# Kernel optimization log

Hardware: AMD Instinct MI355X
Metric: run time of the kernel (lower is better)

## Reference

```python
import jax, jax.numpy as jnp
import numpy as np

B, S, D = 2, 2048, 2048
HQ, HKV = 16, 4
DH = D // HQ            # 128
P = 8192                # GLU projection dim
ROPE_BASE = 10000.0
EPS = 1e-5              # RMSNorm eps


def setup_inputs() -> dict:
    key = jax.random.key(0)
    ks = jax.random.split(key, 9)
    def w(k, shape, scale=0.02):
        return jax.random.normal(k, shape, jnp.float32) * scale
    x = jax.random.normal(ks[0], (B, S, D), jnp.float32)
    # additive causal mask: 0 on/below diagonal, -1e9 above
    causal = jnp.where(jnp.tril(jnp.ones((S, S), bool)), 0.0, -1e9).astype(jnp.float32)
    return dict(
        x=x,
        attention_mask=causal,
        Wq=w(ks[1], (D, D)),
        Wk=w(ks[2], (D, HKV * DH)),
        Wv=w(ks[3], (D, HKV * DH)),
        Wo=w(ks[4], (D, D)),
        Wg=w(ks[5], (D, P)), bg=jnp.zeros((P,), jnp.float32),
        Wu=w(ks[6], (D, P)), bu=jnp.zeros((P,), jnp.float32),
        Wd=w(ks[7], (P, D)), bd=jnp.zeros((D,), jnp.float32),
        g1=jnp.ones((D,), jnp.float32),
        g2=jnp.ones((D,), jnp.float32),
    )


def _rmsnorm(h, g):
    return h * jax.lax.rsqrt(jnp.mean(h * h, axis=-1, keepdims=True) + EPS) * g


def reference(x, attention_mask, Wq, Wk, Wv, Wo, Wg, bg, Wu, bu, Wd, bd, g1, g2):
    b, s, _ = x.shape
    # RoPE tables (half-split / rotate-half convention)
    pos = jnp.arange(s, dtype=jnp.float32)
    inv_freq = ROPE_BASE ** (-jnp.arange(DH // 2, dtype=jnp.float32) * 2.0 / DH)
    ang = pos[:, None] * inv_freq[None, :]          # [s, dh/2]
    cos, sin = jnp.cos(ang), jnp.sin(ang)
    def rope(v):                                    # v: [..., s, dh]
        v1, v2 = jnp.split(v, 2, axis=-1)
        return jnp.concatenate([v1 * cos - v2 * sin, v1 * sin + v2 * cos], axis=-1)

    # --- pre-norm GQA attention sub-block ---
    xn = _rmsnorm(x, g1)
    Q = (xn @ Wq).reshape(b, s, HQ, DH).transpose(0, 2, 1, 3)    # [b,hq,s,dh]
    K = (xn @ Wk).reshape(b, s, HKV, DH).transpose(0, 2, 1, 3)   # [b,g,s,dh]
    V = (xn @ Wv).reshape(b, s, HKV, DH).transpose(0, 2, 1, 3)   # [b,g,s,dh]
    Q, K = rope(Q), rope(K)
    # split q heads: (head group) with group = HKV, head varies slowest
    Qg = Q.reshape(b, HQ // HKV, HKV, s, DH)                     # [b,h,g,s,dh]
    scores = jnp.einsum('bhgsd,bgtd->bhgst', Qg, K) / np.float32(np.sqrt(DH))
    scores = scores + attention_mask                             # broadcast [s,t]
    att = jax.nn.softmax(scores, axis=-1)
    o = jnp.einsum('bhgst,bgtd->bhgsd', att, V)                  # [b,h,g,s,dh]
    o = o.transpose(0, 3, 1, 2, 4).reshape(b, s, D)              # (head group dhead)
    h = x + o @ Wo

    # --- pre-norm GLU (SwiGLU) feedforward sub-block ---
    hn = _rmsnorm(h, g2)
    glu = (jax.nn.silu(hn @ Wg + bg) * (hn @ Wu + bu)) @ Wd + bd
    return h + glu
```

## Files before the change

kernel.cpp:

```cpp
#include <hip/hip_runtime.h>
#include <hip/hip_bf16.h>
#include <stdint.h>

#define S_LEN 2048
#define NROW  4096
#define DQKV  3072

typedef unsigned short u16;
typedef __attribute__((ext_vector_type(8))) short bf16x8;
typedef __attribute__((ext_vector_type(4))) float f32x4;

__device__ __forceinline__ float bf2f(u16 v) {
  unsigned int u = ((unsigned int)v) << 16;
  return __builtin_bit_cast(float, u);
}
__device__ __forceinline__ u16 f2bf(float f) {
  unsigned int u = __builtin_bit_cast(unsigned int, f);
  u += 0x7FFFu + ((u >> 16) & 1u);
  return (u16)(u >> 16);
}
__device__ __forceinline__ void async16(const void* g, void* l) {
  __builtin_amdgcn_global_load_lds(
      (const __attribute__((address_space(1))) unsigned int*)(uintptr_t)g,
      (__attribute__((address_space(3))) unsigned int*)(uintptr_t)l, 16, 0, 0);
}

__global__ __launch_bounds__(256) void transpose_f32_bf16(
    const float* __restrict__ in, u16* __restrict__ out, int R, int C) {
  __shared__ float t[32][33];
  const int bx = blockIdx.x * 32;
  const int by = blockIdx.y * 32;
  const int tx = threadIdx.x, ty = threadIdx.y;
#pragma unroll
  for (int i = 0; i < 32; i += 8)
    t[ty + i][tx] = in[(size_t)(by + ty + i) * C + bx + tx];
  __syncthreads();
#pragma unroll
  for (int i = 0; i < 32; i += 8)
    out[(size_t)(bx + ty + i) * R + by + tx] = f2bf(t[tx][ty + i]);
}

__global__ __launch_bounds__(256) void rope_tables(float* __restrict__ cosT,
                                                   float* __restrict__ sinT) {
  int idx = blockIdx.x * 256 + threadIdx.x;
  int i = idx & 63, s = idx >> 6;
  float inv = powf(10000.0f, -2.0f * (float)i / 128.0f);
  float ang = (float)s * inv;
  cosT[idx] = cosf(ang);
  sinT[idx] = sinf(ang);
}

__global__ __launch_bounds__(256) void rope_apply(u16* __restrict__ QKV,
                                                  const float* __restrict__ cosT,
                                                  const float* __restrict__ sinT) {
  int idx = blockIdx.x * 256 + threadIdx.x;
  int i = idx & 63;
  int h20 = (idx >> 6) % 20;
  int row = idx / (64 * 20);
  int s = row & (S_LEN - 1);
  int col = (h20 < 16) ? (h20 * 128) : (2048 + (h20 - 16) * 128);
  size_t base = (size_t)row * DQKV + col;
  float v1 = bf2f(QKV[base + i]);
  float v2 = bf2f(QKV[base + 64 + i]);
  float c = cosT[s * 64 + i], sn = sinT[s * 64 + i];
  QKV[base + i]      = f2bf(v1 * c - v2 * sn);
  QKV[base + 64 + i] = f2bf(v1 * sn + v2 * c);
}

__global__ __launch_bounds__(256) void rmsnorm_kernel(const float* __restrict__ x,
                                                      const float* __restrict__ g,
                                                      u16* __restrict__ out) {
  const int row = blockIdx.x, tid = threadIdx.x;
  const float* xr = x + (size_t)row * 2048;
  float4 a = ((const float4*)xr)[tid * 2];
  float4 b = ((const float4*)xr)[tid * 2 + 1];
  float ss = a.x*a.x + a.y*a.y + a.z*a.z + a.w*a.w
           + b.x*b.x + b.y*b.y + b.z*b.z + b.w*b.w;
#pragma unroll
  for (int m = 1; m < 64; m <<= 1) ss += __shfl_xor(ss, m, 64);
  __shared__ float red[4];
  if ((tid & 63) == 0) red[tid >> 6] = ss;
  __syncthreads();
  float tot = red[0] + red[1] + red[2] + red[3];
  float rms = rsqrtf(tot * (1.0f / 2048.0f) + 1e-5f);
  const int c = tid * 8;
  float v[8] = {a.x,a.y,a.z,a.w,b.x,b.y,b.z,b.w};
  u16 o[8];
#pragma unroll
  for (int j = 0; j < 8; j++) o[j] = f2bf(v[j] * rms * g[c + j]);
  *(uint4*)(out + (size_t)row * 2048 + c) = *(uint4*)o;
}

template <int BN, int MODE>
__global__ __launch_bounds__(512, 2) void gemm256(
    const u16* __restrict__ A, const u16* __restrict__ Bt,
    int nx, int K, int N,
    const float* __restrict__ bias, const float* __restrict__ res,
    u16* __restrict__ outb, float* __restrict__ outf) {
  constexpr int BSLOT = (BN == 256) ? 16384 : 8192;
  constexpr int NF = BN / 64;
  __shared__ char ldsA[4 * 16384] __attribute__((aligned(16)));
  __shared__ char ldsB[4 * BSLOT] __attribute__((aligned(16)));
  const int t = threadIdx.x;
  const int nwg = gridDim.x;
  const int wg = ((int)blockIdx.x & 7) * (nwg >> 3) + ((int)blockIdx.x >> 3);
  const int m0 = (wg / nx) * 256, n0 = (wg % nx) * BN;
  const int l = t & 63, w = t >> 6;
  const int wm = w >> 2, wn = w & 3;
  const int lr = l & 15, lg = l >> 4;

  const int cA  = (t & 7) ^ ((t >> 3) & 7);
  const int rb  = 2 * (t >> 3) + (cA >> 2);
  const int kcb = (cA & 3) * 16;
  const int t16 = t * 16;
  const char* aS0 = (const char*)A  + ((size_t)(m0 + rb) * K) * 2 + kcb;
  const char* aS1 = aS0 + (size_t)128 * K * 2;
  const char* bS0 = (const char*)Bt + ((size_t)(n0 + rb) * K) * 2 + kcb;
  const char* bS1 = bS0 + (size_t)128 * K * 2;

  const int NT = K >> 5;

  auto STAGE = [&](int kt) {
    const int slot = kt & 3;
    const size_t ko = (size_t)kt * 64;
    char* sA = ldsA + slot * 16384;
    async16(aS0 + ko, sA + t16);
    async16(aS1 + ko, sA + 8192 + t16);
    char* sB = ldsB + slot * BSLOT;
    async16(bS0 + ko, sB + t16);
    if constexpr (BN == 256) async16(bS1 + ko, sB + 8192 + t16);
  };

  STAGE(0); STAGE(1); STAGE(2);

  f32x4 acc[8][NF] = {};
  const int ci  = ((lg + ((lr & 1) << 2)) ^ ((lr >> 1) & 7)) << 4;
  const int aRd = (wm * 64 + (lr >> 1)) * 128 + ci;
  const int bRd = ((BN == 256 ? wn * 32 : wn * 16) + (lr >> 1)) * 128 + ci;

  for (int kt = 0; kt < NT; ++kt) {
    if (kt < NT - 2) {
      if constexpr (BN == 256) asm volatile("s_waitcnt vmcnt(8)" ::: "memory");
      else                     asm volatile("s_waitcnt vmcnt(6)" ::: "memory");
    } else if (kt == NT - 2) {
      if constexpr (BN == 256) asm volatile("s_waitcnt vmcnt(4)" ::: "memory");
      else                     asm volatile("s_waitcnt vmcnt(3)" ::: "memory");
    } else {
      asm volatile("s_waitcnt vmcnt(0)" ::: "memory");
    }
    __builtin_amdgcn_sched_barrier(0);
    __builtin_amdgcn_s_barrier();
    __builtin_amdgcn_sched_barrier(0);
    if (kt + 3 < NT) STAGE(kt + 3);
    const char* sA = ldsA + (kt & 3) * 16384;
    const char* sB = ldsB + (kt & 3) * BSLOT;
    bf16x8 aF[8], bF[NF];
#pragma unroll
    for (int m = 0; m < 8; m++) aF[m] = *(const bf16x8*)(sA + aRd + m * 1024);
#pragma unroll
    for (int n = 0; n < NF; n++) bF[n] = *(const bf16x8*)(sB + bRd + n * 1024);
    __builtin_amdgcn_s_setprio(1);
#pragma unroll
    for (int m = 0; m < 8; m++)
#pragma unroll
      for (int n = 0; n < NF; n++)
        acc[m][n] = __builtin_amdgcn_mfma_f32_16x16x32_bf16(aF[m], bF[n], acc[m][n], 0, 0, 0);
    __builtin_amdgcn_s_setprio(0);
  }

#pragma unroll
  for (int m = 0; m < 8; m++) {
    const int row = m0 + wm * 128 + m * 16 + lg * 4;
#pragma unroll
    for (int n = 0; n < NF; n++) {
      const int col = n0 + wn * (BN / 4) + n * 16 + lr;
      const float bv = bias ? bias[col] : 0.0f;
#pragma unroll
      for (int r = 0; r < 4; r++) {
        const size_t idx = (size_t)(row + r) * N + col;
        float v = acc[m][n][r] + bv;
        if (MODE == 0) outb[idx] = f2bf(v);
        else           outf[idx] = v + res[idx];
      }
    }
  }
}

__global__ __launch_bounds__(512, 2) void swiglu_gemm(
    const u16* __restrict__ A, const u16* __restrict__ Bg, const u16* __restrict__ Bu,
    int nx, int K, const float* __restrict__ bgv, const float* __restrict__ buv,
    u16* __restrict__ out) {
  __shared__ char ldsA[4 * 16384] __attribute__((aligned(16)));
  __shared__ char ldsB[4 * 16384] __attribute__((aligned(16)));
  const int t = threadIdx.x;
  const int nwg = gridDim.x;
  const int wg = ((int)blockIdx.x & 7) * (nwg >> 3) + ((int)blockIdx.x >> 3);
  const int m0 = (wg / nx) * 256, n0 = (wg % nx) * 128;
  const int l = t & 63, w = t >> 6;
  const int wm = w >> 2, wn = w & 3;
  const int lr = l & 15, lg = l >> 4;

  const int cA  = (t & 7) ^ ((t >> 3) & 7);
  const int rb  = 2 * (t >> 3) + (cA >> 2);
  const int kcb = (cA & 3) * 16;
  const int t16 = t * 16;
  const char* aS0 = (const char*)A  + ((size_t)(m0 + rb) * K) * 2 + kcb;
  const char* aS1 = aS0 + (size_t)128 * K * 2;
  const char* gS  = (const char*)Bg + ((size_t)(n0 + rb) * K) * 2 + kcb;
  const char* uS  = (const char*)Bu + ((size_t)(n0 + rb) * K) * 2 + kcb;

  const int NT = K >> 5;

  auto STAGE = [&](int kt) {
    const int slot = kt & 3;
    const size_t ko = (size_t)kt * 64;
    char* sA = ldsA + slot * 16384;
    async16(aS0 + ko, sA + t16);
    async16(aS1 + ko, sA + 8192 + t16);
    char* sB = ldsB + slot * 16384;
    async16(gS + ko, sB + t16);
    async16(uS + ko, sB + 8192 + t16);
  };

  STAGE(0); STAGE(1); STAGE(2);

  f32x4 accg[8][2] = {}, accu[8][2] = {};
  const int ci  = ((lg + ((lr & 1) << 2)) ^ ((lr >> 1) & 7)) << 4;
  const int aRd = (wm * 64 + (lr >> 1)) * 128 + ci;
  const int bRd = (wn * 16 + (lr >> 1)) * 128 + ci;

  for (int kt = 0; kt < NT; ++kt) {
    if (kt < NT - 2)       asm volatile("s_waitcnt vmcnt(8)" ::: "memory");
    else if (kt == NT - 2) asm volatile("s_waitcnt vmcnt(4)" ::: "memory");
    else                   asm volatile("s_waitcnt vmcnt(0)" ::: "memory");
    __builtin_amdgcn_sched_barrier(0);
    __builtin_amdgcn_s_barrier();
    __builtin_amdgcn_sched_barrier(0);
    if (kt + 3 < NT) STAGE(kt + 3);
    const char* sA = ldsA + (kt & 3) * 16384;
    const char* sB = ldsB + (kt & 3) * 16384;
    bf16x8 aF[8], gF[2], uF[2];
#pragma unroll
    for (int m = 0; m < 8; m++) aF[m] = *(const bf16x8*)(sA + aRd + m * 1024);
#pragma unroll
    for (int n = 0; n < 2; n++) {
      gF[n] = *(const bf16x8*)(sB + bRd + n * 1024);
      uF[n] = *(const bf16x8*)(sB + 8192 + bRd + n * 1024);
    }
    __builtin_amdgcn_s_setprio(1);
#pragma unroll
    for (int m = 0; m < 8; m++)
#pragma unroll
      for (int n = 0; n < 2; n++) {
        accg[m][n] = __builtin_amdgcn_mfma_f32_16x16x32_bf16(aF[m], gF[n], accg[m][n], 0, 0, 0);
        accu[m][n] = __builtin_amdgcn_mfma_f32_16x16x32_bf16(aF[m], uF[n], accu[m][n], 0, 0, 0);
      }
    __builtin_amdgcn_s_setprio(0);
  }

#pragma unroll
  for (int m = 0; m < 8; m++) {
    const int row = m0 + wm * 128 + m * 16 + lg * 4;
#pragma unroll
    for (int n = 0; n < 2; n++) {
      const int col = n0 + wn * 32 + n * 16 + lr;
      const float bgc = bgv[col], buc = buv[col];
#pragma unroll
      for (int r = 0; r < 4; r++) {
        float gv = accg[m][n][r] + bgc;
        float uv = accu[m][n][r] + buc;
        float sg = gv / (1.0f + __expf(-gv));
        out[(size_t)(row + r) * 8192 + col] = f2bf(sg * uv);
      }
    }
  }
}

__global__ __launch_bounds__(256) void attn_kernel(const u16* __restrict__ QKV,
                                                   u16* __restrict__ O) {
  const int bid = blockIdx.x;
  const int half = bid >> 8, rr = bid & 255;
  const int bh = rr >> 3, tt = rr & 7;
  const int qtile = half ? (15 - tt) : tt;
  const int b = bh >> 4, hq = bh & 15, g = hq & 3;
  const int q0 = qtile * 128;
  const int tid = threadIdx.x, l = tid & 63, w = tid >> 6;
  const int lr = l & 15, lg = l >> 4;

  __shared__ u16 kT[64 * 128] __attribute__((aligned(16)));
  __shared__ u16 vT[128 * 64] __attribute__((aligned(16)));
  __shared__ u16 pT[4][32 * 72] __attribute__((aligned(16)));

  const float scale = 0.08838834764831845f;

  bf16x8 qF[2][4];
  const int qrow_base = b * S_LEN + q0 + w * 32;
#pragma unroll
  for (int mq = 0; mq < 2; mq++)
#pragma unroll
    for (int kk = 0; kk < 4; kk++)
      qF[mq][kk] = *(const bf16x8*)(QKV + (size_t)(qrow_base + mq * 16 + lr) * DQKV
                                    + hq * 128 + kk * 32 + lg * 8);

  f32x4 o_acc[2][8] = {};
  float m_run[2][4], l_run[2][4];
#pragma unroll
  for (int mq = 0; mq < 2; mq++)
#pragma unroll
    for (int r = 0; r < 4; r++) { m_run[mq][r] = -1e30f; l_run[mq][r] = 0.0f; }

  const int qmin_w = q0 + w * 32;
  const int nt = (q0 + 128) >> 6;

  for (int it = 0; it < nt; ++it) {
    const int t0 = it * 64;
    __syncthreads();
    {
      const int rbase = tid >> 3;
      const int c16 = (tid & 7) * 16;
#pragma unroll
      for (int pass = 0; pass < 2; ++pass) {
        const int r = rbase + pass * 32;
        const u16* src = QKV + (size_t)(b * S_LEN + t0 + r) * DQKV + 2048 + g * 128 + c16;
        const int rk = r & 7;
#pragma unroll
        for (int jj = 0; jj < 2; ++jj) {
          bf16x8 kv = *(const bf16x8*)(src + jj * 8);
          const int chunk = (c16 >> 3) + jj;
          *(bf16x8*)&kT[r * 128 + ((chunk ^ rk) << 3)] = kv;
        }
#pragma unroll
        for (int jj = 0; jj < 2; ++jj) {
          bf16x8 vv = *(const bf16x8*)(src + 512 + jj * 8);
#pragma unroll
          for (int j = 0; j < 8; ++j) {
            const int d = c16 + jj * 8 + j;
            const int key = (d ^ (d >> 4)) & 7;
            vT[d * 64 + (r & 7) + (((r >> 3) ^ key) << 3)] = (u16)vv[j];
          }
        }
      }
    }
    __syncthreads();

    if (t0 <= qmin_w + 31) {
      f32x4 sc[2][4] = {};
#pragma unroll
      for (int mt = 0; mt < 4; mt++) {
        const int tq = mt * 16 + lr;
        const int tk = tq & 7;
#pragma unroll
        for (int kk = 0; kk < 4; kk++) {
          bf16x8 kF = *(const bf16x8*)&kT[tq * 128 + (((kk * 4 + lg) ^ tk) << 3)];
          sc[0][mt] = __builtin_amdgcn_mfma_f32_16x16x32_bf16(qF[0][kk], kF, sc[0][mt], 0, 0, 0);
          sc[1][mt] = __builtin_amdgcn_mfma_f32_16x16x32_bf16(qF[1][kk], kF, sc[1][mt], 0, 0, 0);
        }
      }
      const bool needMask = (t0 + 63 > qmin_w);
#pragma unroll
      for (int mq = 0; mq < 2; mq++)
#pragma unroll
        for (int mt = 0; mt < 4; mt++)
#pragma unroll
          for (int r = 0; r < 4; r++) {
            float v = sc[mq][mt][r] * scale;
            if (needMask) {
              int qg = qmin_w + mq * 16 + lg * 4 + r;
              int tg = t0 + mt * 16 + lr;
              if (tg > qg) v = -1e30f;
            }
            sc[mq][mt][r] = v;
          }
#pragma unroll
      for (int mq = 0; mq < 2; mq++) {
        float al[4];
#pragma unroll
        for (int r = 0; r < 4; r++) {
          float tmax = fmaxf(fmaxf(sc[mq][0][r], sc[mq][1][r]),
                             fmaxf(sc[mq][2][r], sc[mq][3][r]));
#pragma unroll
          for (int m = 1; m < 16; m <<= 1) tmax = fmaxf(tmax, __shfl_xor(tmax, m, 64));
          float mn = fmaxf(m_run[mq][r], tmax);
          float a = __expf(m_run[mq][r] - mn);
          m_run[mq][r] = mn;
          float rs = 0.0f;
#pragma unroll
          for (int mt = 0; mt < 4; mt++) {
            float pv = __expf(sc[mq][mt][r] - mn);
            sc[mq][mt][r] = pv;
            rs += pv;
          }
#pragma unroll
          for (int m = 1; m < 16; m <<= 1) rs += __shfl_xor(rs, m, 64);
          l_run[mq][r] = l_run[mq][r] * a + rs;
          al[r] = a;
        }
#pragma unroll
        for (int n = 0; n < 8; n++)
#pragma unroll
          for (int r = 0; r < 4; r++) o_acc[mq][n][r] *= al[r];
#pragma unroll
        for (int mt = 0; mt < 4; mt++)
#pragma unroll
          for (int r = 0; r < 4; r++)
            pT[w][(mq * 16 + lg * 4 + r) * 72 + mt * 16 + lr] = f2bf(sc[mq][mt][r]);
      }
      bf16x8 pF[2][2];
#pragma unroll
      for (int mq = 0; mq < 2; mq++)
#pragma unroll
        for (int kt = 0; kt < 2; kt++)
          pF[mq][kt] = *(const bf16x8*)&pT[w][(mq * 16 + lr) * 72 + kt * 32 + lg * 8];
#pragma unroll
      for (int kt = 0; kt < 2; kt++)
#pragma unroll
        for (int n = 0; n < 8; n++) {
          const int d = n * 16 + lr;
          const int key = (d ^ (d >> 4)) & 7;
          bf16x8 vF = *(const bf16x8*)&vT[d * 64 + (((kt * 4 + lg) ^ key) << 3)];
          o_acc[0][n] = __builtin_amdgcn_mfma_f32_16x16x32_bf16(pF[0][kt], vF, o_acc[0][n], 0, 0, 0);
          o_acc[1][n] = __builtin_amdgcn_mfma_f32_16x16x32_bf16(pF[1][kt], vF, o_acc[1][n], 0, 0, 0);
        }
    }
  }
#pragma unroll
  for (int mq = 0; mq < 2; mq++)
#pragma unroll
    for (int n = 0; n < 8; n++)
#pragma unroll
      for (int r = 0; r < 4; r++) {
        float v = o_acc[mq][n][r] / l_run[mq][r];
        int row = b * S_LEN + q0 + w * 32 + mq * 16 + lg * 4 + r;
        int col = hq * 128 + n * 16 + lr;
        O[(size_t)row * 2048 + col] = f2bf(v);
      }
}

extern "C" void kernel_launch(void* const* d_in, const int* in_sizes, int n_in,
                              void* d_out, int out_size, void* d_ws, size_t ws_size,
                              hipStream_t stream) {
  const float* x  = (const float*)d_in[0];
  const float* Wq = (const float*)d_in[2];
  const float* Wk = (const float*)d_in[3];
  const float* Wv = (const float*)d_in[4];
  const float* Wo = (const float*)d_in[5];
  const float* Wg = (const float*)d_in[6];
  const float* bg = (const float*)d_in[7];
  const float* Wu = (const float*)d_in[8];
  const float* bu = (const float*)d_in[9];
  const float* Wd = (const float*)d_in[10];
  const float* bd = (const float*)d_in[11];
  const float* g1 = (const float*)d_in[12];
  const float* g2 = (const float*)d_in[13];

  char* p = (char*)d_ws;
  auto alloc = [&](size_t bytes) { char* r = p; p += (bytes + 255) & ~(size_t)255; return r; };
  u16*   BtQKV = (u16*)alloc((size_t)DQKV * 2048 * 2);
  u16*   WoT   = (u16*)alloc((size_t)2048 * 2048 * 2);
  u16*   WgT   = (u16*)alloc((size_t)8192 * 2048 * 2);
  u16*   WuT   = (u16*)alloc((size_t)8192 * 2048 * 2);
  u16*   WdT   = (u16*)alloc((size_t)2048 * 8192 * 2);
  u16*   xn    = (u16*)alloc((size_t)NROW * 2048 * 2);
  u16*   QKV   = (u16*)alloc((size_t)NROW * DQKV * 2);
  u16*   Obuf  = (u16*)alloc((size_t)NROW * 2048 * 2);
  float* h     = (float*)alloc((size_t)NROW * 2048 * 4);
  u16*   gact  = (u16*)alloc((size_t)NROW * 8192 * 2);
  float* cosT  = (float*)alloc((size_t)S_LEN * 64 * 4);
  float* sinT  = (float*)alloc((size_t)S_LEN * 64 * 4);

  dim3 tb(32, 8);
  transpose_f32_bf16<<<dim3(2048/32, 2048/32), tb, 0, stream>>>(Wq, BtQKV,                    2048, 2048);
  transpose_f32_bf16<<<dim3( 512/32, 2048/32), tb, 0, stream>>>(Wk, BtQKV + 2048ull*2048,     2048,  512);
  transpose_f32_bf16<<<dim3( 512/32, 2048/32), tb, 0, stream>>>(Wv, BtQKV + 2560ull*2048,     2048,  512);
  transpose_f32_bf16<<<dim3(2048/32, 2048/32), tb, 0, stream>>>(Wo, WoT,                      2048, 2048);
  transpose_f32_bf16<<<dim3(8192/32, 2048/32), tb, 0, stream>>>(Wg, WgT,                      2048, 8192);
  transpose_f32_bf16<<<dim3(8192/32, 2048/32), tb, 0, stream>>>(Wu, WuT,                      2048, 8192);
  transpose_f32_bf16<<<dim3(2048/32, 8192/32), tb, 0, stream>>>(Wd, WdT,                      8192, 2048);

  rope_tables<<<(S_LEN * 64) / 256, 256, 0, stream>>>(cosT, sinT);

  rmsnorm_kernel<<<NROW, 256, 0, stream>>>(x, g1, xn);

  gemm256<256, 0><<<192, 512, 0, stream>>>(xn, BtQKV, 12, 2048, 3072,
                                           nullptr, nullptr, QKV, nullptr);

  rope_apply<<<(NROW * 20 * 64) / 256, 256, 0, stream>>>(QKV, cosT, sinT);

  attn_kernel<<<512, 256, 0, stream>>>(QKV, Obuf);

  gemm256<128, 1><<<256, 512, 0, stream>>>(Obuf, WoT, 16, 2048, 2048,
                                           nullptr, x, nullptr, h);

  rmsnorm_kernel<<<NROW, 256, 0, stream>>>(h, g2, xn);

  swiglu_gemm<<<1024, 512, 0, stream>>>(xn, WgT, WuT, 64, 2048, bg, bu, gact);

  gemm256<128, 1><<<256, 512, 0, stream>>>(gact, WdT, 16, 8192, 2048,
                                           bd, h, nullptr, (float*)d_out);
}
```

Measured before the change: 829.0 us.

## Restructure GEMM main loops into 8-phase ping-pong pipeline with K=64 tiles

Replaces the 4-slot K=32 software pipeline in the dense and SwiGLU GEMMs with a double-buffered K=64 scheme. Each iteration is split into four phases that interleave LDS fragment reads, barriers, partial async global-to-LDS loads, and MFMA blocks. The aim is to overlap memory traffic with compute more finely and cut per-iteration wait overhead. In exchange it adds many more workgroup barriers per iteration, and the wrap-around prefetch indices load unused data on the final iterations.

Result: no change. 829.3 us (+0.0%).

```diff
diff --git a/kernel.cpp b/kernel.cpp
--- a/kernel.cpp
+++ b/kernel.cpp
@@ -24,6 +24,11 @@
       (const __attribute__((address_space(1))) unsigned int*)(uintptr_t)g,
       (__attribute__((address_space(3))) unsigned int*)(uintptr_t)l, 16, 0, 0);
 }
+#define LGKM0  do { asm volatile("s_waitcnt lgkmcnt(0)" ::: "memory"); \
+                    __builtin_amdgcn_sched_barrier(0); } while (0)
+#define VMC(n) do { asm volatile("s_waitcnt vmcnt(" #n ")" ::: "memory"); \
+                    __builtin_amdgcn_sched_barrier(0); } while (0)
+#define BAR()  __builtin_amdgcn_s_barrier()
 
 __global__ __launch_bounds__(256) void transpose_f32_bf16(
     const float* __restrict__ in, u16* __restrict__ out, int R, int C) {
@@ -92,15 +97,15 @@
 }
 
 template <int BN, int MODE>
-__global__ __launch_bounds__(512, 2) void gemm256(
+__global__ __launch_bounds__(512, 2) void gemm8p(
     const u16* __restrict__ A, const u16* __restrict__ Bt,
     int nx, int K, int N,
     const float* __restrict__ bias, const float* __restrict__ res,
     u16* __restrict__ outb, float* __restrict__ outf) {
-  constexpr int BSLOT = (BN == 256) ? 16384 : 8192;
   constexpr int NF = BN / 64;
-  __shared__ char ldsA[4 * 16384] __attribute__((aligned(16)));
-  __shared__ char ldsB[4 * BSLOT] __attribute__((aligned(16)));
+  constexpr int BB = BN * 128;
+  __shared__ char ldsA[2 * 32768] __attribute__((aligned(16)));
+  __shared__ char ldsB[2 * BB]    __attribute__((aligned(16)));
   const int t = threadIdx.x;
   const int nwg = gridDim.x;
   const int wg = ((int)blockIdx.x & 7) * (nwg >> 3) + ((int)blockIdx.x >> 3);
@@ -109,63 +114,106 @@
   const int wm = w >> 2, wn = w & 3;
   const int lr = l & 15, lg = l >> 4;
 
-  const int cA  = (t & 7) ^ ((t >> 3) & 7);
-  const int rb  = 2 * (t >> 3) + (cA >> 2);
-  const int kcb = (cA & 3) * 16;
+  const size_t K2 = (size_t)K * 2;
+  const int pr = t >> 3;
+  const int ckb = ((t & 7) ^ (pr & 7)) * 16;
   const int t16 = t * 16;
-  const char* aS0 = (const char*)A  + ((size_t)(m0 + rb) * K) * 2 + kcb;
-  const char* aS1 = aS0 + (size_t)128 * K * 2;
-  const char* bS0 = (const char*)Bt + ((size_t)(n0 + rb) * K) * 2 + kcb;
-  const char* bS1 = bS0 + (size_t)128 * K * 2;
-
-  const int NT = K >> 5;
-
-  auto STAGE = [&](int kt) {
-    const int slot = kt & 3;
-    const size_t ko = (size_t)kt * 64;
-    char* sA = ldsA + slot * 16384;
-    async16(aS0 + ko, sA + t16);
-    async16(aS1 + ko, sA + 8192 + t16);
-    char* sB = ldsB + slot * BSLOT;
-    async16(bS0 + ko, sB + t16);
-    if constexpr (BN == 256) async16(bS1 + ko, sB + 8192 + t16);
+  const char* aSrc = (const char*)A  + (size_t)(m0 + pr) * K2 + ckb;
+  const char* bSrc = (const char*)Bt + (size_t)(n0 + pr) * K2 + ckb;
+
+  auto ST_A = [&](int q, int kt, int buf) {
+    char* d = ldsA + buf * 32768 + q * 16384 + t16;
+    const char* s = aSrc + (size_t)(q * 128) * K2 + (size_t)kt * 128;
+    async16(s, d);
+    async16(s + (size_t)64 * K2, d + 8192);
   };
-
-  STAGE(0); STAGE(1); STAGE(2);
+  auto ST_B = [&](int h, int kt, int buf) {
+    if constexpr (BN == 256) {
+      char* d = ldsB + buf * 32768 + h * 16384 + t16;
+      const char* s = bSrc + (size_t)(h * 128) * K2 + (size_t)kt * 128;
+      async16(s, d);
+      async16(s + (size_t)64 * K2, d + 8192);
+    } else {
+      char* d = ldsB + buf * 16384 + h * 8192 + t16;
+      const char* s = bSrc + (size_t)(h * 64) * K2 + (size_t)kt * 128;
+      async16(s, d);
+    }
+  };
+
+  const int NT = K >> 6;
+  ST_A(0, 0, 0); ST_A(1, 0, 0); ST_B(0, 0, 0); ST_B(1, 0, 0);
+  ST_A(0, 1, 1); ST_A(1, 1, 1);
+  VMC(4);
+  BAR();
+
+  const int key = lr & 7;
+  const int c0 = (lg ^ key) * 16;
+  const int c1 = ((4 + lg) ^ key) * 16;
+  const int aB = wm * 16384 + lr * 128;
+  const int bB = (BN == 256) ? ((wn >> 1) * 16384 + ((wn & 1) * 64 + lr) * 128)
+                             : ((wn >> 1) * 8192  + ((wn & 1) * 32 + lr) * 128);
 
   f32x4 acc[8][NF] = {};
-  const int ci  = ((lg + ((lr & 1) << 2)) ^ ((lr >> 1) & 7)) << 4;
-  const int aRd = (wm * 64 + (lr >> 1)) * 128 + ci;
-  const int bRd = ((BN == 256 ? wn * 32 : wn * 16) + (lr >> 1)) * 128 + ci;
 
   for (int kt = 0; kt < NT; ++kt) {
-    if (kt < NT - 2) {
-      if constexpr (BN == 256) asm volatile("s_waitcnt vmcnt(8)" ::: "memory");
-      else                     asm volatile("s_waitcnt vmcnt(6)" ::: "memory");
-    } else if (kt == NT - 2) {
-      if constexpr (BN == 256) asm volatile("s_waitcnt vmcnt(4)" ::: "memory");
-      else                     asm volatile("s_waitcnt vmcnt(3)" ::: "memory");
-    } else {
-      asm volatile("s_waitcnt vmcnt(0)" ::: "memory");
-    }
-    __builtin_amdgcn_sched_barrier(0);
-    __builtin_amdgcn_s_barrier();
-    __builtin_amdgcn_sched_barrier(0);
-    if (kt + 3 < NT) STAGE(kt + 3);
-    const char* sA = ldsA + (kt & 3) * 16384;
-    const char* sB = ldsB + (kt & 3) * BSLOT;
-    bf16x8 aF[8], bF[NF];
-#pragma unroll
-    for (int m = 0; m < 8; m++) aF[m] = *(const bf16x8*)(sA + aRd + m * 1024);
-#pragma unroll
-    for (int n = 0; n < NF; n++) bF[n] = *(const bf16x8*)(sB + bRd + n * 1024);
-    __builtin_amdgcn_s_setprio(1);
-#pragma unroll
-    for (int m = 0; m < 8; m++)
+    const int bufc = kt & 1, bufn = bufc ^ 1;
+    const int t1 = (kt + 1 < NT) ? kt + 1 : 0;
+    const int t2 = (kt + 2 < NT) ? kt + 2 : kt + 2 - NT;
+    const char* sA = ldsA + bufc * 32768;
+    const char* sB = ldsB + bufc * BB;
+    bf16x8 aF0[8], aF1[8], bF0[NF], bF1[NF];
+#pragma unroll
+    for (int m = 0; m < 8; m++) aF0[m] = *(const bf16x8*)(sA + aB + m * 2048 + c0);
+#pragma unroll
+    for (int n = 0; n < NF; n++) bF0[n] = *(const bf16x8*)(sB + bB + n * 2048 + c0);
+    LGKM0;
+    BAR();
+    ST_B(0, t1, bufn);
+    __builtin_amdgcn_s_setprio(1);
+#pragma unroll
+    for (int m = 0; m < 4; m++)
 #pragma unroll
       for (int n = 0; n < NF; n++)
-        acc[m][n] = __builtin_amdgcn_mfma_f32_16x16x32_bf16(aF[m], bF[n], acc[m][n], 0, 0, 0);
-    __builtin_amdgcn_s_setprio(0);
+        acc[m][n] = __builtin_amdgcn_mfma_f32_16x16x32_bf16(aF0[m], bF0[n], acc[m][n], 0, 0, 0);
+    __builtin_amdgcn_s_setprio(0);
+    BAR();
+#pragma unroll
+    for (int m = 0; m < 8; m++) aF1[m] = *(const bf16x8*)(sA + aB + m * 2048 + c1);
+    LGKM0;
+    BAR();
+    ST_B(1, t1, bufn);
+    __builtin_amdgcn_s_setprio(1);
+#pragma unroll
+    for (int m = 4; m < 8; m++)
+#pragma unroll
+      for (int n = 0; n < NF; n++)
+        acc[m][n] = __builtin_amdgcn_mfma_f32_16x16x32_bf16(aF0[m], bF0[n], acc[m][n], 0, 0, 0);
+    __builtin_amdgcn_s_setprio(0);
+    BAR();
+#pragma unroll
+    for (int n = 0; n < NF; n++) bF1[n] = *(const bf16x8*)(sB + bB + n * 2048 + c1);
+    LGKM0;
+    BAR();
+    ST_A(0, t2, bufc);
+    __builtin_amdgcn_s_setprio(1);
+#pragma unroll
+    for (int m = 0; m < 4; m++)
+#pragma unroll
+      for (int n = 0; n < NF; n++)
+        acc[m][n] = __builtin_amdgcn_mfma_f32_16x16x32_bf16(aF1[m], bF1[n], acc[m][n], 0, 0, 0);
+    __builtin_amdgcn_s_setprio(0);
+    BAR();
+    VMC(2);
+    BAR();
+    ST_A(1, t2, bufc);
+    __builtin_amdgcn_s_setprio(1);
+#pragma unroll
+    for (int m = 4; m < 8; m++)
+#pragma unroll
+      for (int n = 0; n < NF; n++)
+        acc[m][n] = __builtin_amdgcn_mfma_f32_16x16x32_bf16(aF1[m], bF1[n], acc[m][n], 0, 0, 0);
+    __builtin_amdgcn_s_setprio(0);
+    BAR();
   }
 
 #pragma unroll
@@ -186,12 +234,12 @@
   }
 }
 
-__global__ __launch_bounds__(512, 2) void swiglu_gemm(
+__global__ __launch_bounds__(512, 2) void swiglu8p(
     const u16* __restrict__ A, const u16* __restrict__ Bg, const u16* __restrict__ Bu,
     int nx, int K, const float* __restrict__ bgv, const float* __restrict__ buv,
     u16* __restrict__ out) {
-  __shared__ char ldsA[4 * 16384] __attribute__((aligned(16)));
-  __shared__ char ldsB[4 * 16384] __attribute__((aligned(16)));
+  __shared__ char ldsA[2 * 32768] __attribute__((aligned(16)));
+  __shared__ char ldsB[2 * 32768] __attribute__((aligned(16)));
   const int t = threadIdx.x;
   const int nwg = gridDim.x;
   const int wg = ((int)blockIdx.x & 7) * (nwg >> 3) + ((int)blockIdx.x >> 3);
@@ -200,62 +248,106 @@
   const int wm = w >> 2, wn = w & 3;
   const int lr = l & 15, lg = l >> 4;
 
-  const int cA  = (t & 7) ^ ((t >> 3) & 7);
-  const int rb  = 2 * (t >> 3) + (cA >> 2);
-  const int kcb = (cA & 3) * 16;
+  const size_t K2 = (size_t)K * 2;
+  const int pr = t >> 3;
+  const int ckb = ((t & 7) ^ (pr & 7)) * 16;
   const int t16 = t * 16;
-  const char* aS0 = (const char*)A  + ((size_t)(m0 + rb) * K) * 2 + kcb;
-  const char* aS1 = aS0 + (size_t)128 * K * 2;
-  const char* gS  = (const char*)Bg + ((size_t)(n0 + rb) * K) * 2 + kcb;
-  const char* uS  = (const char*)Bu + ((size_t)(n0 + rb) * K) * 2 + kcb;
-
-  const int NT = K >> 5;
-
-  auto STAGE = [&](int kt) {
-    const int slot = kt & 3;
-    const size_t ko = (size_t)kt * 64;
-    char* sA = ldsA + slot * 16384;
-    async16(aS0 + ko, sA + t16);
-    async16(aS1 + ko, sA + 8192 + t16);
-    char* sB = ldsB + slot * 16384;
-    async16(gS + ko, sB + t16);
-    async16(uS + ko, sB + 8192 + t16);
+  const char* aSrc = (const char*)A  + (size_t)(m0 + pr) * K2 + ckb;
+  const char* gSrc = (const char*)Bg + (size_t)(n0 + pr) * K2 + ckb;
+  const char* uSrc = (const char*)Bu + (size_t)(n0 + pr) * K2 + ckb;
+
+  auto ST_A = [&](int q, int kt, int buf) {
+    char* d = ldsA + buf * 32768 + q * 16384 + t16;
+    const char* s = aSrc + (size_t)(q * 128) * K2 + (size_t)kt * 128;
+    async16(s, d);
+    async16(s + (size_t)64 * K2, d + 8192);
   };
-
-  STAGE(0); STAGE(1); STAGE(2);
+  auto ST_GU = [&](int h, int kt, int buf) {
+    char* d = ldsB + buf * 32768 + h * 16384 + t16;
+    const char* s = (h ? uSrc : gSrc) + (size_t)kt * 128;
+    async16(s, d);
+    async16(s + (size_t)64 * K2, d + 8192);
+  };
+
+  const int NT = K >> 6;
+  ST_A(0, 0, 0); ST_A(1, 0, 0); ST_GU(0, 0, 0); ST_GU(1, 0, 0);
+  ST_A(0, 1, 1); ST_A(1, 1, 1);
+  VMC(4);
+  BAR();
+
+  const int key = lr & 7;
+  const int c0 = (lg ^ key) * 16;
+  const int c1 = ((4 + lg) ^ key) * 16;
+  const int aB = wm * 16384 + lr * 128;
+  const int gB = (wn * 32 + lr) * 128;
 
   f32x4 accg[8][2] = {}, accu[8][2] = {};
-  const int ci  = ((lg + ((lr & 1) << 2)) ^ ((lr >> 1) & 7)) << 4;
-  const int aRd = (wm * 64 + (lr >> 1)) * 128 + ci;
-  const int bRd = (wn * 16 + (lr >> 1)) * 128 + ci;
 
   for (int kt = 0; kt < NT; ++kt) {
-    if (kt < NT - 2)       asm volatile("s_waitcnt vmcnt(8)" ::: "memory");
-    else if (kt == NT - 2) asm volatile("s_waitcnt vmcnt(4)" ::: "memory");
-    else                   asm volatile("s_waitcnt vmcnt(0)" ::: "memory");
-    __builtin_amdgcn_sched_barrier(0);
-    __builtin_amdgcn_s_barrier();
-    __builtin_amdgcn_sched_barrier(0);
-    if (kt + 3 < NT) STAGE(kt + 3);
-    const char* sA = ldsA + (kt & 3) * 16384;
-    const char* sB = ldsB + (kt & 3) * 16384;
-    bf16x8 aF[8], gF[2], uF[2];
-#pragma unroll
-    for (int m = 0; m < 8; m++) aF[m] = *(const bf16x8*)(sA + aRd + m * 1024);
+    const int bufc = kt & 1, bufn = bufc ^ 1;
+    const int t1 = (kt + 1 < NT) ? kt + 1 : 0;
+    const int t2 = (kt + 2 < NT) ? kt + 2 : kt + 2 - NT;
+    const char* sA = ldsA + bufc * 32768;
+    const char* sB = ldsB + bufc * 32768;
+    bf16x8 aF0[8], aF1[8], gF0[2], gF1[2], uF0[2], uF1[2];
+#pragma unroll
+    for (int m = 0; m < 8; m++) aF0[m] = *(const bf16x8*)(sA + aB + m * 2048 + c0);
 #pragma unroll
     for (int n = 0; n < 2; n++) {
-      gF[n] = *(const bf16x8*)(sB + bRd + n * 1024);
-      uF[n] = *(const bf16x8*)(sB + 8192 + bRd + n * 1024);
-    }
+      gF0[n] = *(const bf16x8*)(sB + gB + n * 2048 + c0);
+      uF0[n] = *(const bf16x8*)(sB + 16384 + gB + n * 2048 + c0);
+    }
+    LGKM0;
+    BAR();
+    ST_GU(0, t1, bufn);
     __builtin_amdgcn_s_setprio(1);
 #pragma unroll
     for (int m = 0; m < 8; m++)
 #pragma unroll
-      for (int n = 0; n < 2; n++) {
-        accg[m][n] = __builtin_amdgcn_mfma_f32_16x16x32_bf16(aF[m], gF[n], accg[m][n], 0, 0, 0);
-        accu[m][n] = __builtin_amdgcn_mfma_f32_16x16x32_bf16(aF[m], uF[n], accu[m][n], 0, 0, 0);
-      }
-    __builtin_amdgcn_s_setprio(0);
+      for (int n = 0; n < 2; n++)
+        accg[m][n] = __builtin_amdgcn_mfma_f32_16x16x32_bf16(aF0[m], gF0[n], accg[m][n], 0, 0, 0);
+    __builtin_amdgcn_s_setprio(0);
+    BAR();
+#pragma unroll
+    for (int m = 0; m < 8; m++) aF1[m] = *(const bf16x8*)(sA + aB + m * 2048 + c1);
+    LGKM0;
+    BAR();
+    ST_GU(1, t1, bufn);
+    __builtin_amdgcn_s_setprio(1);
+#pragma unroll
+    for (int m = 0; m < 8; m++)
+#pragma unroll
+      for (int n = 0; n < 2; n++)
+        accu[m][n] = __builtin_amdgcn_mfma_f32_16x16x32_bf16(aF0[m], uF0[n], accu[m][n], 0, 0, 0);
+    __builtin_amdgcn_s_setprio(0);
+    BAR();
+#pragma unroll
+    for (int n = 0; n < 2; n++) {
+      gF1[n] = *(const bf16x8*)(sB + gB + n * 2048 + c1);
+      uF1[n] = *(const bf16x8*)(sB + 16384 + gB + n * 2048 + c1);
+    }
+    LGKM0;
+    BAR();
+    ST_A(0, t2, bufc);
+    __builtin_amdgcn_s_setprio(1);
+#pragma unroll
+    for (int m = 0; m < 8; m++)
+#pragma unroll
+      for (int n = 0; n < 2; n++)
+        accg[m][n] = __builtin_amdgcn_mfma_f32_16x16x32_bf16(aF1[m], gF1[n], accg[m][n], 0, 0, 0);
+    __builtin_amdgcn_s_setprio(0);
+    BAR();
+    VMC(2);
+    BAR();
+    ST_A(1, t2, bufc);
+    __builtin_amdgcn_s_setprio(1);
+#pragma unroll
+    for (int m = 0; m < 8; m++)
+#pragma unroll
+      for (int n = 0; n < 2; n++)
+        accu[m][n] = __builtin_amdgcn_mfma_f32_16x16x32_bf16(aF1[m], uF1[n], accu[m][n], 0, 0, 0);
+    __builtin_amdgcn_s_setprio(0);
+    BAR();
   }
 
 #pragma unroll
@@ -335,8 +427,8 @@
 #pragma unroll
           for (int j = 0; j < 8; ++j) {
             const int d = c16 + jj * 8 + j;
-            const int key = (d ^ (d >> 4)) & 7;
-            vT[d * 64 + (r & 7) + (((r >> 3) ^ key) << 3)] = (u16)vv[j];
+            const int keyv = (d ^ (d >> 4)) & 7;
+            vT[d * 64 + (r & 7) + (((r >> 3) ^ keyv) << 3)] = (u16)vv[j];
           }
         }
       }
@@ -409,17 +501,17 @@
 #pragma unroll
       for (int mq = 0; mq < 2; mq++)
 #pragma unroll
-        for (int kt = 0; kt < 2; kt++)
-          pF[mq][kt] = *(const bf16x8*)&pT[w][(mq * 16 + lr) * 72 + kt * 32 + lg * 8];
-#pragma unroll
-      for (int kt = 0; kt < 2; kt++)
+        for (int ktp = 0; ktp < 2; ktp++)
+          pF[mq][ktp] = *(const bf16x8*)&pT[w][(mq * 16 + lr) * 72 + ktp * 32 + lg * 8];
+#pragma unroll
+      for (int ktp = 0; ktp < 2; ktp++)
 #pragma unroll
         for (int n = 0; n < 8; n++) {
           const int d = n * 16 + lr;
-          const int key = (d ^ (d >> 4)) & 7;
-          bf16x8 vF = *(const bf16x8*)&vT[d * 64 + (((kt * 4 + lg) ^ key) << 3)];
-          o_acc[0][n] = __builtin_amdgcn_mfma_f32_16x16x32_bf16(pF[0][kt], vF, o_acc[0][n], 0, 0, 0);
-          o_acc[1][n] = __builtin_amdgcn_mfma_f32_16x16x32_bf16(pF[1][kt], vF, o_acc[1][n], 0, 0, 0);
+          const int keyv = (d ^ (d >> 4)) & 7;
+          bf16x8 vF = *(const bf16x8*)&vT[d * 64 + (((ktp * 4 + lg) ^ keyv) << 3)];
+          o_acc[0][n] = __builtin_amdgcn_mfma_f32_16x16x32_bf16(pF[0][ktp], vF, o_acc[0][n], 0, 0, 0);
+          o_acc[1][n] = __builtin_amdgcn_mfma_f32_16x16x32_bf16(pF[1][ktp], vF, o_acc[1][n], 0, 0, 0);
         }
     }
   }
@@ -469,32 +561,32 @@
   float* sinT  = (float*)alloc((size_t)S_LEN * 64 * 4);
 
   dim3 tb(32, 8);
-  transpose_f32_bf16<<<dim3(2048/32, 2048/32), tb, 0, stream>>>(Wq, BtQKV,                    2048, 2048);
-  transpose_f32_bf16<<<dim3( 512/32, 2048/32), tb, 0, stream>>>(Wk, BtQKV + 2048ull*2048,     2048,  512);
-  transpose_f32_bf16<<<dim3( 512/32, 2048/32), tb, 0, stream>>>(Wv, BtQKV + 2560ull*2048,     2048,  512);
-  transpose_f32_bf16<<<dim3(2048/32, 2048/32), tb, 0, stream>>>(Wo, WoT,                      2048, 2048);
-  transpose_f32_bf16<<<dim3(8192/32, 2048/32), tb, 0, stream>>>(Wg, WgT,                      2048, 8192);
-  transpose_f32_bf16<<<dim3(8192/32, 2048/32), tb, 0, stream>>>(Wu, WuT,                      2048, 8192);
-  transpose_f32_bf16<<<dim3(2048/32, 8192/32), tb, 0, stream>>>(Wd, WdT,                      8192, 2048);
+  transpose_f32_bf16<<<dim3(2048/32, 2048/32), tb, 0, stream>>>(Wq, BtQKV,                2048, 2048);
+  transpose_f32_bf16<<<dim3( 512/32, 2048/32), tb, 0, stream>>>(Wk, BtQKV + 2048ull*2048, 2048,  512);
+  transpose_f32_bf16<<<dim3( 512/32, 2048/32), tb, 0, stream>>>(Wv, BtQKV + 2560ull*2048, 2048,  512);
+  transpose_f32_bf16<<<dim3(2048/32, 2048/32), tb, 0, stream>>>(Wo, WoT,                  2048, 2048);
+  transpose_f32_bf16<<<dim3(8192/32, 2048/32), tb, 0, stream>>>(Wg, WgT,                  2048, 8192);
+  transpose_f32_bf16<<<dim3(8192/32, 2048/32), tb, 0, stream>>>(Wu, WuT,                  2048, 8192);
+  transpose_f32_bf16<<<dim3(2048/32, 8192/32), tb, 0, stream>>>(Wd, WdT,                  8192, 2048);
 
   rope_tables<<<(S_LEN * 64) / 256, 256, 0, stream>>>(cosT, sinT);
 
   rmsnorm_kernel<<<NROW, 256, 0, stream>>>(x, g1, xn);
 
-  gemm256<256, 0><<<192, 512, 0, stream>>>(xn, BtQKV, 12, 2048, 3072,
-                                           nullptr, nullptr, QKV, nullptr);
+  gemm8p<256, 0><<<192, 512, 0, stream>>>(xn, BtQKV, 12, 2048, 3072,
+                                          nullptr, nullptr, QKV, nullptr);
 
   rope_apply<<<(NROW * 20 * 64) / 256, 256, 0, stream>>>(QKV, cosT, sinT);
 
   attn_kernel<<<512, 256, 0, stream>>>(QKV, Obuf);
 
-  gemm256<128, 1><<<256, 512, 0, stream>>>(Obuf, WoT, 16, 2048, 2048,
-                                           nullptr, x, nullptr, h);
+  gemm8p<128, 1><<<256, 512, 0, stream>>>(Obuf, WoT, 16, 2048, 2048,
+                                          nullptr, x, nullptr, h);
 
   rmsnorm_kernel<<<NROW, 256, 0, stream>>>(h, g2, xn);
 
-  swiglu_gemm<<<1024, 512, 0, stream>>>(xn, WgT, WuT, 64, 2048, bg, bu, gact);
-
-  gemm256<128, 1><<<256, 512, 0, stream>>>(gact, WdT, 16, 8192, 2048,
-                                           bd, h, nullptr, (float*)d_out);
-}
+  swiglu8p<<<1024, 512, 0, stream>>>(xn, WgT, WuT, 64, 2048, bg, bu, gact);
+
+  gemm8p<128, 1><<<256, 512, 0, stream>>>(gact, WdT, 16, 8192, 2048,
+                                          bd, h, nullptr, (float*)d_out);
+}
```
